# Optimization experiments

Hardware: AMD Instinct MI355X
Metric: run time of the kernel (lower is better)

Reference implementation:

```python
import jax, jax.numpy as jnp
import numpy as np

N_NODES = 50000
N_EDGES = 800000
IN_FEAT = 256
OUT_FEAT = 128
P_EDGE = 0.2   # edge dropout rate
P_NODE = 0.1   # node-feature dropout rate
BN_EPS = 1e-5


def setup_inputs() -> dict:
    key = jax.random.key(0)
    ks = jax.random.split(key, 8)
    features = jax.random.normal(ks[0], (N_NODES, IN_FEAT), dtype=jnp.float32)
    W = jax.random.normal(ks[1], (IN_FEAT, OUT_FEAT), dtype=jnp.float32) / np.sqrt(IN_FEAT)
    b = jnp.zeros((OUT_FEAT,), dtype=jnp.float32)
    gamma = jnp.ones((OUT_FEAT,), dtype=jnp.float32)
    beta = jnp.zeros((OUT_FEAT,), dtype=jnp.float32)
    src = jax.random.randint(ks[2], (N_EDGES,), 0, N_NODES, dtype=jnp.int64)
    dst = jax.random.randint(ks[3], (N_EDGES,), 0, N_NODES, dtype=jnp.int64)
    edge_rand = jax.random.uniform(ks[4], (N_EDGES,), dtype=jnp.float32)
    node_rand = jax.random.uniform(ks[5], (N_NODES, OUT_FEAT), dtype=jnp.float32)
    return {"features": features, "W": W, "b": b, "gamma": gamma, "beta": beta,
            "src": src, "dst": dst, "edge_rand": edge_rand, "node_rand": node_rand}


def reference(features, W, b, gamma, beta, src, dst, edge_rand, node_rand):
    dt = features.dtype
    # --- edge dropout: keep-mask over edges (no rescale, per DropEdge convention) ---
    emask = (edge_rand >= P_EDGE).astype(dt)                      # [E]
    # --- GCN conv, norm='both' on the dropped graph ---
    h = features @ W                                              # [N, out] (W first: out < in)
    deg_src = jax.ops.segment_sum(emask, src, num_segments=N_NODES)  # out-degrees
    deg_dst = jax.ops.segment_sum(emask, dst, num_segments=N_NODES)  # in-degrees
    coef = emask * jax.lax.rsqrt(jnp.maximum(deg_src[src], 1.0) * jnp.maximum(deg_dst[dst], 1.0))
    msg = h[src] * coef[:, None]                                  # [E, out]
    agg = jax.ops.segment_sum(msg, dst, num_segments=N_NODES) + b  # [N, out]
    # --- BatchNorm1d (training mode: batch statistics over nodes) ---
    mean = jnp.mean(agg, axis=0)
    var = jnp.var(agg, axis=0)
    y = (agg - mean) * jax.lax.rsqrt(var + BN_EPS) * gamma + beta
    # --- node-feature dropout (inverted scaling) ---
    nmask = (node_rand >= P_NODE).astype(dt) / (1.0 - P_NODE)
    return y * nmask
```

## Files before the change

### kernel.cpp

```cpp
#include <hip/hip_runtime.h>

#define N_NODES 50000
#define N_EDGES 800000
#define IN_FEAT 256
#define OUT_FEAT 128
#define P_EDGE 0.2f
#define P_NODE 0.1f
#define BN_EPS 1e-5f
#define CAP 64
#define GEMM_BLOCKS 782
#define EDGE_BLOCKS 782
#define ZERO_BLOCKS 98
#define PREPW_BLOCKS 128
#define AGG_BLOCKS 1024
#define FIN_BLOCKS 8

typedef __bf16 bf16x8 __attribute__((ext_vector_type(8)));
typedef float floatx4 __attribute__((ext_vector_type(4)));
typedef float f32x4 __attribute__((ext_vector_type(4)));
typedef int i32x4 __attribute__((ext_vector_type(4)));

__device__ inline float bflo(unsigned u) { return __uint_as_float(u << 16); }
__device__ inline float bfhi(unsigned u) { return __uint_as_float(u & 0xffff0000u); }

__global__ __launch_bounds__(256) void k_init(const float* __restrict__ W,
    uint4* __restrict__ zero_base, __bf16* __restrict__ Wt) {
  if (blockIdx.x < ZERO_BLOCKS) {
    int i = blockIdx.x * 256 + threadIdx.x;
    if (i < 25000) zero_base[i] = make_uint4(0u, 0u, 0u, 0u);
  } else {
    int idx = (blockIdx.x - ZERO_BLOCKS) * 256 + threadIdx.x;
    int k = idx >> 7, n = idx & 127;
    Wt[n * IN_FEAT + k] = (__bf16)W[idx];
  }
}

__device__ inline bf16x8 cvt8(f32x4 a, f32x4 b) {
  bf16x8 v;
  v[0] = (__bf16)a[0]; v[1] = (__bf16)a[1]; v[2] = (__bf16)a[2]; v[3] = (__bf16)a[3];
  v[4] = (__bf16)b[0]; v[5] = (__bf16)b[1]; v[6] = (__bf16)b[2]; v[7] = (__bf16)b[3];
  return v;
}

__global__ __launch_bounds__(256) void k_edge(
    const int* __restrict__ src, const int* __restrict__ dst,
    const float* __restrict__ er, unsigned* __restrict__ deg_src,
    unsigned* __restrict__ deg_dst, unsigned short* __restrict__ edge_src) {
  int t = blockIdx.x * 256 + threadIdx.x;
  if (t < N_EDGES / 4) {
    f32x4 e4 = ((const f32x4*)er)[t];
    i32x4 s4 = ((const i32x4*)src)[t];
    i32x4 d4 = ((const i32x4*)dst)[t];
    const bool k0 = e4[0] >= P_EDGE, k1 = e4[1] >= P_EDGE;
    const bool k2 = e4[2] >= P_EDGE, k3 = e4[3] >= P_EDGE;
    if (k0) atomicAdd(&deg_src[s4[0]], 1u);
    if (k1) atomicAdd(&deg_src[s4[1]], 1u);
    if (k2) atomicAdd(&deg_src[s4[2]], 1u);
    if (k3) atomicAdd(&deg_src[s4[3]], 1u);
    unsigned p0 = 0xffffffffu, p1 = 0xffffffffu, p2 = 0xffffffffu, p3 = 0xffffffffu;
    if (k0) p0 = atomicAdd(&deg_dst[d4[0]], 1u);
    if (k1) p1 = atomicAdd(&deg_dst[d4[1]], 1u);
    if (k2) p2 = atomicAdd(&deg_dst[d4[2]], 1u);
    if (k3) p3 = atomicAdd(&deg_dst[d4[3]], 1u);
    if (p0 < CAP) edge_src[(unsigned)d4[0] * CAP + p0] = (unsigned short)s4[0];
    if (p1 < CAP) edge_src[(unsigned)d4[1] * CAP + p1] = (unsigned short)s4[1];
    if (p2 < CAP) edge_src[(unsigned)d4[2] * CAP + p2] = (unsigned short)s4[2];
    if (p3 < CAP) edge_src[(unsigned)d4[3] * CAP + p3] = (unsigned short)s4[3];
  }
}

__global__ __launch_bounds__(256, 2) void k_gemm(const float* __restrict__ feat,
    const __bf16* __restrict__ Wt, __bf16* __restrict__ h) {
  __shared__ char lds[65536];
  const int t = threadIdx.x;

  const uint4* wsrc = (const uint4*)Wt;
#pragma unroll
  for (int i = 0; i < 16; i++) {
    int c = i * 256 + t;
    unsigned o = (unsigned)c * 16u;
    unsigned row = o >> 9;
    *(uint4*)(lds + (o ^ ((row & 7u) << 4))) = wsrc[c];
  }
  __syncthreads();

  const int lane = t & 63;
  const int wave = t >> 6;
  const int l16 = lane & 15;
  const int quad = lane >> 4;
  const int m0 = blockIdx.x * 64 + wave * 16;

  int mload = m0 + l16;
  if (mload >= N_NODES) mload = N_NODES - 1;

  bf16x8 a[8];
#pragma unroll
  for (int kk = 0; kk < 8; kk++) {
    const f32x4* p = (const f32x4*)(feat + (size_t)mload * IN_FEAT + kk * 32 + quad * 8);
    a[kk] = cvt8(p[0], p[1]);
  }

  floatx4 acc[8];
#pragma unroll
  for (int g = 0; g < 8; g++) {
    const unsigned row = (unsigned)(g * 16 + l16);
    const unsigned base = row * 512u + (unsigned)quad * 16u;
    const unsigned swz = (row & 7u) << 4;
    floatx4 c = {0.f, 0.f, 0.f, 0.f};
#pragma unroll
    for (int kk = 0; kk < 8; kk++) {
      bf16x8 b = *(const bf16x8*)(lds + ((base + (unsigned)kk * 64u) ^ swz));
      c = __builtin_amdgcn_mfma_f32_16x16x32_bf16(a[kk], b, c, 0, 0, 0);
    }
    acc[g] = c;
  }
  __syncthreads();

  char* hb = lds + wave * 16384;
#pragma unroll
  for (int g = 0; g < 8; g++) {
#pragma unroll
    for (int r = 0; r < 4; r++) {
      unsigned row = (unsigned)(quad * 4 + r);
      unsigned o = row * 256u + (unsigned)(g * 16 + l16) * 2u;
      *(__bf16*)(hb + (o ^ ((row & 7u) << 4))) = (__bf16)acc[g][r];
    }
  }
#pragma unroll
  for (int j = 0; j < 4; j++) {
    unsigned row = (unsigned)(lane >> 4) + (unsigned)j * 4u;
    unsigned o = row * 256u + (unsigned)(lane & 15) * 16u;
    uint4 v = *(const uint4*)(hb + (o ^ ((row & 7u) << 4)));
    int grow = m0 + (int)row;
    if (grow < N_NODES)
      *(uint4*)((char*)h + (size_t)grow * 256 + (size_t)(lane & 15) * 16) = v;
  }
}

__global__ __launch_bounds__(256) void k_agg(const unsigned short* __restrict__ h,
    const unsigned short* __restrict__ edge_src, const unsigned* __restrict__ deg_src,
    const unsigned* __restrict__ deg_dst, const float* __restrict__ bias,
    float* __restrict__ out, float* __restrict__ psum, float* __restrict__ pssq) {
  const int wid = threadIdx.x >> 6;
  const int lane = threadIdx.x & 63;
  const int g = lane >> 4;
  const int cl = lane & 15;
  const int wave_global = blockIdx.x * 4 + wid;

  float b8[8];
#pragma unroll
  for (int j = 0; j < 8; j++) b8[j] = bias[cl * 8 + j];

  float s8[8], ss8[8];
#pragma unroll
  for (int j = 0; j < 8; j++) { s8[j] = 0.f; ss8[j] = 0.f; }

  for (int d = wave_global; d < N_NODES; d += AGG_BLOCKS * 4) {
    const unsigned cnt = deg_dst[d];
    unsigned lim = cnt > CAP ? CAP : cnt;
    const unsigned base = (unsigned)d * CAP;
    float acc[8];
#pragma unroll
    for (int j = 0; j < 8; j++) acc[j] = 0.f;

#pragma unroll 4
    for (unsigned i = 0; i < lim; i += 4) {
      unsigned e = i + (unsigned)g;
      bool valid = e < lim;
      unsigned idx = (unsigned)edge_src[base + (valid ? e : 0u)];
      unsigned dg = deg_src[idx];
      float r = valid ? rsqrtf((float)(dg ? dg : 1u)) : 0.f;
      uint4 u = *(const uint4*)(h + (size_t)idx * OUT_FEAT + cl * 8);
      acc[0] = fmaf(bflo(u.x), r, acc[0]);
      acc[1] = fmaf(bfhi(u.x), r, acc[1]);
      acc[2] = fmaf(bflo(u.y), r, acc[2]);
      acc[3] = fmaf(bfhi(u.y), r, acc[3]);
      acc[4] = fmaf(bflo(u.z), r, acc[4]);
      acc[5] = fmaf(bfhi(u.z), r, acc[5]);
      acc[6] = fmaf(bflo(u.w), r, acc[6]);
      acc[7] = fmaf(bfhi(u.w), r, acc[7]);
    }
#pragma unroll
    for (int j = 0; j < 8; j++) {
      acc[j] += __shfl_xor(acc[j], 16);
      acc[j] += __shfl_xor(acc[j], 32);
    }
    if (g == 0) {
      float sc = rsqrtf((float)(cnt ? cnt : 1u));
      float o[8];
#pragma unroll
      for (int j = 0; j < 8; j++) {
        o[j] = fmaf(acc[j], sc, b8[j]);
        s8[j] += o[j];
        ss8[j] = fmaf(o[j], o[j], ss8[j]);
      }
      float4 o0 = make_float4(o[0], o[1], o[2], o[3]);
      float4 o1 = make_float4(o[4], o[5], o[6], o[7]);
      *(float4*)(out + (size_t)d * OUT_FEAT + cl * 8) = o0;
      *(float4*)(out + (size_t)d * OUT_FEAT + cl * 8 + 4) = o1;
    }
  }

  __shared__ float ls[4][16][8], lss[4][16][8];
  if (g == 0) {
#pragma unroll
    for (int j = 0; j < 8; j++) { ls[wid][cl][j] = s8[j]; lss[wid][cl][j] = ss8[j]; }
  }
  __syncthreads();
  if (threadIdx.x < 128) {
    int pcl = threadIdx.x >> 3, pj = threadIdx.x & 7;
    float t = ls[0][pcl][pj] + ls[1][pcl][pj] + ls[2][pcl][pj] + ls[3][pcl][pj];
    float t2 = lss[0][pcl][pj] + lss[1][pcl][pj] + lss[2][pcl][pj] + lss[3][pcl][pj];
    psum[blockIdx.x * OUT_FEAT + threadIdx.x] = t;
    pssq[blockIdx.x * OUT_FEAT + threadIdx.x] = t2;
  }
}

__global__ __launch_bounds__(256) void k_fin(const float* __restrict__ psum,
    const float* __restrict__ pssq, const float* __restrict__ gamma,
    const float* __restrict__ beta, float* __restrict__ a_coef,
    float* __restrict__ b_coef) {
  const int col16 = threadIdx.x & 15;
  const int slice = threadIdx.x >> 4;
  const int c = blockIdx.x * 16 + col16;
  float t = 0.f, t2 = 0.f;
  for (int b = slice; b < AGG_BLOCKS; b += 16) {
    t += psum[b * OUT_FEAT + c];
    t2 += pssq[b * OUT_FEAT + c];
  }
  __shared__ float S[16][17], S2[16][17];
  S[slice][col16] = t;
  S2[slice][col16] = t2;
  __syncthreads();
  if (threadIdx.x < 16) {
    float ts = 0.f, tss = 0.f;
#pragma unroll
    for (int s = 0; s < 16; s++) { ts += S[s][threadIdx.x]; tss += S2[s][threadIdx.x]; }
    int cc = blockIdx.x * 16 + threadIdx.x;
    float mean = ts * (1.0f / N_NODES);
    float var = tss * (1.0f / N_NODES) - mean * mean;
    float a = gamma[cc] * rsqrtf(var + BN_EPS);
    a_coef[cc] = a;
    b_coef[cc] = fmaf(-mean, a, beta[cc]);
  }
}

__global__ __launch_bounds__(256) void k_norm(float* __restrict__ out,
    const float* __restrict__ node_rand, const float* __restrict__ a_coef,
    const float* __restrict__ b_coef) {
  const size_t total4 = (size_t)N_NODES * OUT_FEAT / 4;
  size_t i = (size_t)blockIdx.x * 256 + threadIdx.x;
  if (i < total4) {
    int c0 = (int)((i * 4) & 127);
    f32x4 v = ((const f32x4*)out)[i];
    f32x4 nr = ((const f32x4*)node_rand)[i];
    f32x4 a = *(const f32x4*)(a_coef + c0);
    f32x4 b = *(const f32x4*)(b_coef + c0);
    const float inv = 1.0f / (1.0f - P_NODE);
    f32x4 o;
    o[0] = (nr[0] >= P_NODE ? inv : 0.f) * fmaf(v[0], a[0], b[0]);
    o[1] = (nr[1] >= P_NODE ? inv : 0.f) * fmaf(v[1], a[1], b[1]);
    o[2] = (nr[2] >= P_NODE ? inv : 0.f) * fmaf(v[2], a[2], b[2]);
    o[3] = (nr[3] >= P_NODE ? inv : 0.f) * fmaf(v[3], a[3], b[3]);
    ((f32x4*)out)[i] = o;
  }
}

extern "C" void kernel_launch(void* const* d_in, const int* in_sizes, int n_in,
                              void* d_out, int out_size, void* d_ws, size_t ws_size,
                              hipStream_t stream) {
  const float* feat  = (const float*)d_in[0];
  const float* W     = (const float*)d_in[1];
  const float* bias  = (const float*)d_in[2];
  const float* gamma = (const float*)d_in[3];
  const float* beta  = (const float*)d_in[4];
  const int*   src   = (const int*)d_in[5];
  const int*   dst   = (const int*)d_in[6];
  const float* er    = (const float*)d_in[7];
  const float* nr    = (const float*)d_in[8];
  float* out = (float*)d_out;

  char* ws = (char*)d_ws;
  __bf16*         h        = (__bf16*)        (ws + 0);
  unsigned short* edge_src = (unsigned short*)(ws + 12800000);
  __bf16*         Wt       = (__bf16*)        (ws + 19200000);
  unsigned*       deg_src  = (unsigned*)      (ws + 19265536);
  unsigned*       deg_dst  = (unsigned*)      (ws + 19465536);
  float*          psum     = (float*)         (ws + 19665536);
  float*          pssq     = (float*)         (ws + 20189824);
  float*          a_coef   = (float*)         (ws + 20714112);
  float*          b_coef   = (float*)         (ws + 20714624);

  k_init<<<ZERO_BLOCKS + PREPW_BLOCKS, 256, 0, stream>>>(
      W, (uint4*)(ws + 19265536), Wt);
  k_edge<<<EDGE_BLOCKS, 256, 0, stream>>>(src, dst, er, deg_src, deg_dst, edge_src);
  k_gemm<<<GEMM_BLOCKS, 256, 0, stream>>>(feat, Wt, h);
  k_agg<<<AGG_BLOCKS, 256, 0, stream>>>((const unsigned short*)h, edge_src,
      deg_src, deg_dst, bias, out, psum, pssq);
  k_fin<<<FIN_BLOCKS, 256, 0, stream>>>(psum, pssq, gamma, beta, a_coef, b_coef);
  k_norm<<<(N_NODES * OUT_FEAT / 4 + 255) / 256, 256, 0, stream>>>(out, nr, a_coef, b_coef);
}
```

Before: 282.7 us.

## Partition edge bucketing into eight per-block-group copies with merged degree tables

Result: no change. 287.0 us (+1.5%).

```diff
diff --git a/kernel.cpp b/kernel.cpp
--- a/kernel.cpp
+++ b/kernel.cpp
@@ -7,11 +7,14 @@
 #define P_EDGE 0.2f
 #define P_NODE 0.1f
 #define BN_EPS 1e-5f
-#define CAP 64
+#define NPART 8
+#define CAP_Q 24
+#define PART_STRIDE 1200000
 #define GEMM_BLOCKS 782
 #define EDGE_BLOCKS 782
-#define ZERO_BLOCKS 98
+#define ZERO_BLOCKS 782
 #define PREPW_BLOCKS 128
+#define MERGE_BLOCKS 196
 #define AGG_BLOCKS 1024
 #define FIN_BLOCKS 8
 
@@ -27,7 +30,7 @@
     uint4* __restrict__ zero_base, __bf16* __restrict__ Wt) {
   if (blockIdx.x < ZERO_BLOCKS) {
     int i = blockIdx.x * 256 + threadIdx.x;
-    if (i < 25000) zero_base[i] = make_uint4(0u, 0u, 0u, 0u);
+    if (i < 200000) zero_base[i] = make_uint4(0u, 0u, 0u, 0u);
   } else {
     int idx = (blockIdx.x - ZERO_BLOCKS) * 256 + threadIdx.x;
     int k = idx >> 7, n = idx & 127;
@@ -44,8 +47,12 @@
 
 __global__ __launch_bounds__(256) void k_edge(
     const int* __restrict__ src, const int* __restrict__ dst,
-    const float* __restrict__ er, unsigned* __restrict__ deg_src,
-    unsigned* __restrict__ deg_dst, unsigned short* __restrict__ edge_src) {
+    const float* __restrict__ er, unsigned* __restrict__ deg_src_q,
+    unsigned* __restrict__ deg_dst_q, unsigned short* __restrict__ parts) {
+  const int q = blockIdx.x & 7;
+  unsigned* dsq = deg_src_q + q * N_NODES;
+  unsigned* ddq = deg_dst_q + q * N_NODES;
+  unsigned short* pq = parts + (size_t)q * PART_STRIDE;
   int t = blockIdx.x * 256 + threadIdx.x;
   if (t < N_EDGES / 4) {
     f32x4 e4 = ((const f32x4*)er)[t];
@@ -53,19 +60,42 @@
     i32x4 d4 = ((const i32x4*)dst)[t];
     const bool k0 = e4[0] >= P_EDGE, k1 = e4[1] >= P_EDGE;
     const bool k2 = e4[2] >= P_EDGE, k3 = e4[3] >= P_EDGE;
-    if (k0) atomicAdd(&deg_src[s4[0]], 1u);
-    if (k1) atomicAdd(&deg_src[s4[1]], 1u);
-    if (k2) atomicAdd(&deg_src[s4[2]], 1u);
-    if (k3) atomicAdd(&deg_src[s4[3]], 1u);
     unsigned p0 = 0xffffffffu, p1 = 0xffffffffu, p2 = 0xffffffffu, p3 = 0xffffffffu;
-    if (k0) p0 = atomicAdd(&deg_dst[d4[0]], 1u);
-    if (k1) p1 = atomicAdd(&deg_dst[d4[1]], 1u);
-    if (k2) p2 = atomicAdd(&deg_dst[d4[2]], 1u);
-    if (k3) p3 = atomicAdd(&deg_dst[d4[3]], 1u);
-    if (p0 < CAP) edge_src[(unsigned)d4[0] * CAP + p0] = (unsigned short)s4[0];
-    if (p1 < CAP) edge_src[(unsigned)d4[1] * CAP + p1] = (unsigned short)s4[1];
-    if (p2 < CAP) edge_src[(unsigned)d4[2] * CAP + p2] = (unsigned short)s4[2];
-    if (p3 < CAP) edge_src[(unsigned)d4[3] * CAP + p3] = (unsigned short)s4[3];
+    if (k0) p0 = atomicAdd(&ddq[d4[0]], 1u);
+    if (k1) p1 = atomicAdd(&ddq[d4[1]], 1u);
+    if (k2) p2 = atomicAdd(&ddq[d4[2]], 1u);
+    if (k3) p3 = atomicAdd(&ddq[d4[3]], 1u);
+    if (k0) atomicAdd(&dsq[s4[0]], 1u);
+    if (k1) atomicAdd(&dsq[s4[1]], 1u);
+    if (k2) atomicAdd(&dsq[s4[2]], 1u);
+    if (k3) atomicAdd(&dsq[s4[3]], 1u);
+    if (p0 < CAP_Q) pq[(unsigned)d4[0] * CAP_Q + p0] = (unsigned short)s4[0];
+    if (p1 < CAP_Q) pq[(unsigned)d4[1] * CAP_Q + p1] = (unsigned short)s4[1];
+    if (p2 < CAP_Q) pq[(unsigned)d4[2] * CAP_Q + p2] = (unsigned short)s4[2];
+    if (p3 < CAP_Q) pq[(unsigned)d4[3] * CAP_Q + p3] = (unsigned short)s4[3];
+  }
+}
+
+__global__ __launch_bounds__(256) void k_merge(const unsigned* __restrict__ deg_src_q,
+    const unsigned* __restrict__ deg_dst_q, unsigned long long* __restrict__ cnt8,
+    unsigned char* __restrict__ tot8, unsigned char* __restrict__ deg_src_m) {
+  int n = blockIdx.x * 256 + threadIdx.x;
+  if (n < N_NODES) {
+    unsigned ts = 0;
+#pragma unroll
+    for (int q = 0; q < NPART; q++) ts += deg_src_q[q * N_NODES + n];
+    deg_src_m[n] = (unsigned char)(ts > 255u ? 255u : ts);
+    unsigned long long pack = 0;
+    unsigned tt = 0;
+#pragma unroll
+    for (int q = 0; q < NPART; q++) {
+      unsigned c = deg_dst_q[q * N_NODES + n];
+      tt += c;
+      c = c > CAP_Q ? CAP_Q : c;
+      pack |= (unsigned long long)c << (8 * q);
+    }
+    cnt8[n] = pack;
+    tot8[n] = (unsigned char)(tt > 255u ? 255u : tt);
   }
 }
 
@@ -138,9 +168,10 @@
 }
 
 __global__ __launch_bounds__(256) void k_agg(const unsigned short* __restrict__ h,
-    const unsigned short* __restrict__ edge_src, const unsigned* __restrict__ deg_src,
-    const unsigned* __restrict__ deg_dst, const float* __restrict__ bias,
-    float* __restrict__ out, float* __restrict__ psum, float* __restrict__ pssq) {
+    const unsigned short* __restrict__ parts, const unsigned char* __restrict__ deg_src_m,
+    const unsigned long long* __restrict__ cnt8, const unsigned char* __restrict__ tot8,
+    const float* __restrict__ bias, float* __restrict__ out,
+    float* __restrict__ psum, float* __restrict__ pssq) {
   const int wid = threadIdx.x >> 6;
   const int lane = threadIdx.x & 63;
   const int g = lane >> 4;
@@ -156,19 +187,32 @@
   for (int j = 0; j < 8; j++) { s8[j] = 0.f; ss8[j] = 0.f; }
 
   for (int d = wave_global; d < N_NODES; d += AGG_BLOCKS * 4) {
-    const unsigned cnt = deg_dst[d];
-    unsigned lim = cnt > CAP ? CAP : cnt;
-    const unsigned base = (unsigned)d * CAP;
+    const unsigned long long c8 = cnt8[d];
+    unsigned P[8];
+    unsigned run = 0;
+#pragma unroll
+    for (int q = 0; q < 8; q++) { P[q] = run; run += (unsigned)((c8 >> (8 * q)) & 0xffull); }
+    const unsigned lim = run;
+    const unsigned dbase = (unsigned)d * CAP_Q;
+
     float acc[8];
 #pragma unroll
     for (int j = 0; j < 8; j++) acc[j] = 0.f;
 
-#pragma unroll 4
+#pragma unroll 2
     for (unsigned i = 0; i < lim; i += 4) {
       unsigned e = i + (unsigned)g;
       bool valid = e < lim;
-      unsigned idx = (unsigned)edge_src[base + (valid ? e : 0u)];
-      unsigned dg = deg_src[idx];
+      unsigned ec = valid ? e : 0u;
+      unsigned qq = 0, off = 0;
+#pragma unroll
+      for (int j = 1; j < 8; j++) {
+        bool ge = ec >= P[j];
+        qq += ge ? 1u : 0u;
+        off = ge ? P[j] : off;
+      }
+      unsigned idx = (unsigned)parts[(size_t)qq * PART_STRIDE + dbase + (ec - off)];
+      unsigned dg = deg_src_m[idx];
       float r = valid ? rsqrtf((float)(dg ? dg : 1u)) : 0.f;
       uint4 u = *(const uint4*)(h + (size_t)idx * OUT_FEAT + cl * 8);
       acc[0] = fmaf(bflo(u.x), r, acc[0]);
@@ -186,7 +230,8 @@
       acc[j] += __shfl_xor(acc[j], 32);
     }
     if (g == 0) {
-      float sc = rsqrtf((float)(cnt ? cnt : 1u));
+      unsigned tot = tot8[d];
+      float sc = rsqrtf((float)(tot ? tot : 1u));
       float o[8];
 #pragma unroll
       for (int j = 0; j < 8; j++) {
@@ -281,22 +326,26 @@
   float* out = (float*)d_out;
 
   char* ws = (char*)d_ws;
-  __bf16*         h        = (__bf16*)        (ws + 0);
-  unsigned short* edge_src = (unsigned short*)(ws + 12800000);
-  __bf16*         Wt       = (__bf16*)        (ws + 19200000);
-  unsigned*       deg_src  = (unsigned*)      (ws + 19265536);
-  unsigned*       deg_dst  = (unsigned*)      (ws + 19465536);
-  float*          psum     = (float*)         (ws + 19665536);
-  float*          pssq     = (float*)         (ws + 20189824);
-  float*          a_coef   = (float*)         (ws + 20714112);
-  float*          b_coef   = (float*)         (ws + 20714624);
+  __bf16*             h         = (__bf16*)            (ws + 0);
+  unsigned short*     parts     = (unsigned short*)    (ws + 12800000);
+  __bf16*             Wt        = (__bf16*)            (ws + 32000000);
+  unsigned*           deg_src_q = (unsigned*)          (ws + 32065536);
+  unsigned*           deg_dst_q = (unsigned*)          (ws + 33665536);
+  unsigned long long* cnt8      = (unsigned long long*)(ws + 35265536);
+  unsigned char*      tot8      = (unsigned char*)     (ws + 35665536);
+  unsigned char*      deg_src_m = (unsigned char*)     (ws + 35715584);
+  float*              psum      = (float*)             (ws + 35765760);
+  float*              pssq      = (float*)             (ws + 36290048);
+  float*              a_coef    = (float*)             (ws + 36814336);
+  float*              b_coef    = (float*)             (ws + 36814848);
 
   k_init<<<ZERO_BLOCKS + PREPW_BLOCKS, 256, 0, stream>>>(
-      W, (uint4*)(ws + 19265536), Wt);
-  k_edge<<<EDGE_BLOCKS, 256, 0, stream>>>(src, dst, er, deg_src, deg_dst, edge_src);
+      W, (uint4*)(ws + 32065536), Wt);
+  k_edge<<<EDGE_BLOCKS, 256, 0, stream>>>(src, dst, er, deg_src_q, deg_dst_q, parts);
   k_gemm<<<GEMM_BLOCKS, 256, 0, stream>>>(feat, Wt, h);
-  k_agg<<<AGG_BLOCKS, 256, 0, stream>>>((const unsigned short*)h, edge_src,
-      deg_src, deg_dst, bias, out, psum, pssq);
+  k_merge<<<MERGE_BLOCKS, 256, 0, stream>>>(deg_src_q, deg_dst_q, cnt8, tot8, deg_src_m);
+  k_agg<<<AGG_BLOCKS, 256, 0, stream>>>((const unsigned short*)h, parts,
+      deg_src_m, cnt8, tot8, bias, out, psum, pssq);
   k_fin<<<FIN_BLOCKS, 256, 0, stream>>>(psum, pssq, gamma, beta, a_coef, b_coef);
   k_norm<<<(N_NODES * OUT_FEAT / 4 + 255) / 256, 256, 0, stream>>>(out, nr, a_coef, b_coef);
 }
```
